# Kernel optimization log

Measured on AMD Instinct MI355X. Metric: run time of the kernel, lower is better.

## Reference

```python
import jax, jax.numpy as jnp
import numpy as np

D_MODEL, D_INNER, D_STATE, D_CONV, DT_RANK = 4, 8, 16, 4, 1


def _build_perms(N, H, W):
    # center-out 2D spatial order
    yy, xx = np.meshgrid(np.arange(H), np.arange(W), indexing='ij')
    cy, cx = H // 2, W // 2
    d2 = (yy - cy) ** 2 + (xx - cx) ** 2
    sp = np.argsort(d2.reshape(-1), kind='stable')          # (H*W,)
    HW = H * W
    # scanA: for each frame t, full center-out spatial sweep
    scanA = (np.arange(N)[:, None] * HW + sp[None, :]).reshape(-1)
    # scanB: for each spatial pos (in center-out order), zig-zag over frames
    fwd = np.arange(N)
    bwd = fwd[::-1]
    tids = np.where((np.arange(HW) % 2 == 0)[:, None], fwd[None, :], bwd[None, :])  # (HW, N)
    scanB = (tids * HW + sp[:, None]).reshape(-1)
    perms = np.stack([scanA, scanB, scanA[::-1], scanB[::-1]], axis=0)  # (4, L)
    return jnp.asarray(perms)


def _dwconv1d(x_bcl, w, b, pad, groups):
    # x: (B, C, L), w: (C, 1, K) depthwise
    y = jax.lax.conv_general_dilated(x_bcl, w, (1,), [pad],
                                     feature_group_count=groups,
                                     dimension_numbers=('NCH', 'OIH', 'NCH'))
    return y + b[None, :, None]


def _forward(x, dwconv_w, dwconv_b, in_proj_w, conv1d_w, conv1d_b,
             x_proj_w, dt_proj_w, dt_proj_b, A_log, Dp, out_proj_w, ln_g, ln_b):
    B, N, H, W = x.shape
    L = N * H * W
    perms = _build_perms(N, H, W)                 # (4, L) int, static
    xf = x.reshape(B, L)
    seqs = xf[:, perms]                            # (B, 4, L) gather along 4 scans
    seqs = _dwconv1d(seqs, dwconv_w, dwconv_b, (1, 1), 4)
    u = jax.nn.silu(seqs.transpose(0, 2, 1))       # (B, L, 4)
    # ---- Mamba(d_model=4) ----
    xz = jnp.einsum('bld,ed->ble', u, in_proj_w)   # (B, L, 2*d_inner)
    xm, z = xz[..., :D_INNER], xz[..., D_INNER:]
    xc = _dwconv1d(xm.transpose(0, 2, 1), conv1d_w, conv1d_b, (D_CONV - 1, 0), D_INNER)
    xm = jax.nn.silu(xc.transpose(0, 2, 1))        # (B, L, 8) causal conv + SiLU
    x_dbl = jnp.einsum('bld,ed->ble', xm, x_proj_w)  # (B, L, dt_rank+2*d_state)
    dt = x_dbl[..., :DT_RANK]
    Bm = x_dbl[..., DT_RANK:DT_RANK + D_STATE]     # (B, L, 16)
    Cm = x_dbl[..., DT_RANK + D_STATE:]            # (B, L, 16)
    dt = jax.nn.softplus(jnp.einsum('blr,dr->bld', dt, dt_proj_w) + dt_proj_b)  # (B, L, 8)
    A = -jnp.exp(A_log)                            # (8, 16)
    dA = jnp.exp(dt[..., None] * A)                # (B, L, 8, 16)
    dBx = dt[..., None] * Bm[:, :, None, :] * xm[..., None]  # (B, L, 8, 16)

    def step(h, inp):
        dA_t, dBx_t, C_t = inp
        h = dA_t * h + dBx_t                       # (B, 8, 16)
        return h, jnp.einsum('bds,bs->bd', h, C_t)

    h0 = jnp.zeros((B, D_INNER, D_STATE), x.dtype)
    _, ys = jax.lax.scan(step, h0, (dA.transpose(1, 0, 2, 3),
                                    dBx.transpose(1, 0, 2, 3),
                                    Cm.transpose(1, 0, 2)))
    y = ys.transpose(1, 0, 2) + xm * Dp            # (B, L, 8)
    y = y * jax.nn.silu(z)
    out = jnp.einsum('bld,ed->ble', y, out_proj_w)  # (B, L, 4)
    # ---- LayerNorm(4) ----
    mu = out.mean(-1, keepdims=True)
    var = ((out - mu) ** 2).mean(-1, keepdims=True)
    out = (out - mu) * jax.lax.rsqrt(var + 1e-5) * ln_g + ln_b
    # rec[:, inv[i]] = out[:, :, i]  <=>  rec_i = out[:, perms[i], i]
    rec = jnp.take_along_axis(out, perms.T[None], axis=1)  # (B, L, 4)
    return rec.mean(-1).reshape(B, N, H, W)


def setup_inputs() -> dict:
    key = jax.random.key(0)
    ks = jax.random.split(key, 12)
    s = 0.1
    x = jax.random.normal(ks[0], (4, 6, 128, 128), jnp.float32)
    return {
        'x': x,
        'dwconv_w': jax.random.normal(ks[1], (4, 1, 3), jnp.float32) * s,
        'dwconv_b': jnp.zeros((4,), jnp.float32),
        'in_proj_w': jax.random.normal(ks[2], (2 * D_INNER, D_MODEL), jnp.float32) * s,
        'conv1d_w': jax.random.normal(ks[3], (D_INNER, 1, D_CONV), jnp.float32) * s,
        'conv1d_b': jnp.zeros((D_INNER,), jnp.float32),
        'x_proj_w': jax.random.normal(ks[4], (DT_RANK + 2 * D_STATE, D_INNER), jnp.float32) * s,
        'dt_proj_w': jax.random.normal(ks[5], (D_INNER, DT_RANK), jnp.float32) * s,
        'dt_proj_b': jnp.full((D_INNER,), -2.0, jnp.float32),
        'A_log': jnp.log(jnp.tile(jnp.arange(1, D_STATE + 1, dtype=jnp.float32), (D_INNER, 1))),
        'Dp': jnp.ones((D_INNER,), jnp.float32),
        'out_proj_w': jax.random.normal(ks[6], (D_MODEL, D_INNER), jnp.float32) * s,
        'ln_g': jnp.ones((4,), jnp.float32),
        'ln_b': jnp.zeros((4,), jnp.float32),
    }


def reference(x, dwconv_w, dwconv_b, in_proj_w, conv1d_w, conv1d_b,
              x_proj_w, dt_proj_w, dt_proj_b, A_log, Dp, out_proj_w, ln_g, ln_b):
    return _forward(x, dwconv_w, dwconv_b, in_proj_w, conv1d_w, conv1d_b,
                    x_proj_w, dt_proj_w, dt_proj_b, A_log, Dp, out_proj_w, ln_g, ln_b)
```

## Files before the change

### kernel.cpp

```cpp
#include <hip/hip_runtime.h>
#include <math.h>

#define HWSZ  16384
#define LTOT  98304
#define NB    4
#define TCH   96
#define NCH   1024
#define GCH   64
#define NGRP  16
#define SD    100

__device__ __forceinline__ float siluf(float x){
  return x * __builtin_amdgcn_rcpf(1.f + __expf(-x));
}
__device__ __forceinline__ float softplusf(float x){
  return fmaxf(x, 0.f) + __logf(1.f + __expf(-fabsf(x)));
}

__device__ __forceinline__ float red16(float x){
  int v;
  v = __float_as_int(x);
  x += __int_as_float(__builtin_amdgcn_update_dpp(0, v, 0xB1, 0xF, 0xF, true));
  v = __float_as_int(x);
  x += __int_as_float(__builtin_amdgcn_update_dpp(0, v, 0x4E, 0xF, 0xF, true));
  v = __float_as_int(x);
  x += __int_as_float(__builtin_amdgcn_update_dpp(0, v, 0x141, 0xF, 0xF, true));
  v = __float_as_int(x);
  x += __int_as_float(__builtin_amdgcn_update_dpp(0, v, 0x140, 0xF, 0xF, true));
  return x;
}

__device__ __forceinline__ int rho0(int i, const int* __restrict__ sp){
  int n = i >> 14; int r = i & (HWSZ - 1);
  return (n << 14) + sp[r];
}
__device__ __forceinline__ int rho1(int i, const int* __restrict__ sp){
  unsigned ui = (unsigned)i;
  unsigned r = ui / 6u; unsigned n = ui - r * 6u;
  unsigned t = (r & 1u) ? (5u - n) : n;
  return (int)((t << 14) + (unsigned)sp[r]);
}

__global__ __launch_bounds__(256) void k_rank(int* __restrict__ sp){
  __shared__ int hist[8193];
  __shared__ int part[256];
  const int tid = threadIdx.x;
  for (int v = tid; v < 8193; v += 256) hist[v] = 0;
  __syncthreads();
  for (int jj = tid; jj < HWSZ; jj += 256){
    int dy = (jj >> 7) - 64, dx = (jj & 127) - 64;
    atomicAdd(&hist[dy*dy + dx*dx], 1);
  }
  __syncthreads();
  const int base = tid * 33;
  {
    int sum = 0;
    for (int m = 0; m < 33; ++m){ int v = base + m; if (v < 8193) sum += hist[v]; }
    part[tid] = sum;
  }
  __syncthreads();
  if (tid == 0){
    int run = 0;
    for (int t = 0; t < 256; ++t){ int c = part[t]; part[t] = run; run += c; }
  }
  __syncthreads();
  {
    int run = part[tid];
    for (int m = 0; m < 33; ++m){
      int v = base + m;
      if (v < 8193){ int c = hist[v]; hist[v] = run; run += c; }
    }
  }
  __syncthreads();

  const int j = blockIdx.x * 256 + tid;
  const int y = j >> 7, x = j & 127;
  const int dy = y - 64, dx = x - 64;
  const int v = dy*dy + dx*dx;
  int cnt = hist[v];
  const int r = __float2int_rd(sqrtf((float)v));
  int yp0 = 64 - r; if (yp0 < 0) yp0 = 0;
  int yp1 = 64 + r + 1; if (yp1 > y) yp1 = y;
  for (int yp = yp0; yp < yp1; ++yp){
    int dyp = yp - 64;
    int tt = v - dyp*dyp;
    int rr = __float2int_rn(sqrtf((float)tt));
    if (rr * rr == tt){
      cnt += (rr <= 64) ? 1 : 0;
      cnt += (rr >= 1 && rr <= 63) ? 1 : 0;
    }
  }
  if (x > 64) cnt += 1;
  sp[cnt] = j;
}

__global__ __launch_bounds__(128, 4)
void k_scan(const float* __restrict__ X,
            const float* __restrict__ dww, const float* __restrict__ dwb,
            const float* __restrict__ ipw,
            const float* __restrict__ c1w, const float* __restrict__ c1b,
            const float* __restrict__ xpw,
            const float* __restrict__ dtpw, const float* __restrict__ dtpb,
            const float* __restrict__ Alog,
            const int* __restrict__ sp,
            float* __restrict__ chA, float* __restrict__ chB,
            float* __restrict__ y0g, float4* __restrict__ ug4)
{
  const int c = blockIdx.x, b = blockIdx.y;
  const int c0 = c * TCH;
  const int tid = threadIdx.x;
  const float* Xb = X + (size_t)b * LTOT;

  __shared__ __align__(16) float s_pre[(TCH + 3) * 9];
  __shared__ __align__(16) float s_dt[8 * SD];
  __shared__ __align__(16) float s_dxm[8 * SD];
  __shared__ __align__(16) float s_Bv[16 * SD];
  __shared__ __align__(16) float s_Cv[16 * SD];

  if (tid < TCH + 3){
    const int m = tid;
    const int i = c0 - 3 + m;
    if (i < 0){
      #pragma unroll
      for (int d = 0; d < 8; ++d) s_pre[m*9 + d] = 0.f;
    } else {
      const int i2 = LTOT - 1 - i;
      const bool okm = (i > 0), okp = (i < LTOT - 1);
      int q[12];
      q[0]  = okm ? rho0(i - 1, sp) : 0;
      q[1]  =       rho0(i,     sp);
      q[2]  = okp ? rho0(i + 1, sp) : 0;
      q[3]  = okm ? rho1(i - 1, sp) : 0;
      q[4]  =       rho1(i,     sp);
      q[5]  = okp ? rho1(i + 1, sp) : 0;
      q[6]  = okm ? rho0(i2 + 1, sp) : 0;
      q[7]  =       rho0(i2,     sp);
      q[8]  = okp ? rho0(i2 - 1, sp) : 0;
      q[9]  = okm ? rho1(i2 + 1, sp) : 0;
      q[10] =       rho1(i2,     sp);
      q[11] = okp ? rho1(i2 - 1, sp) : 0;
      float xv[12];
      #pragma unroll
      for (int t = 0; t < 12; ++t) xv[t] = Xb[q[t]];
      if (!okm){ xv[0] = 0.f; xv[3] = 0.f; xv[6] = 0.f; xv[9]  = 0.f; }
      if (!okp){ xv[2] = 0.f; xv[5] = 0.f; xv[8] = 0.f; xv[11] = 0.f; }
      float u[4];
      #pragma unroll
      for (int k = 0; k < 4; ++k){
        float acc = dwb[k];
        acc = fmaf(dww[k*3+0], xv[k*3+0], acc);
        acc = fmaf(dww[k*3+1], xv[k*3+1], acc);
        acc = fmaf(dww[k*3+2], xv[k*3+2], acc);
        u[k] = siluf(acc);
      }
      ug4[(size_t)b * LTOT + i] = make_float4(u[0], u[1], u[2], u[3]);
      #pragma unroll
      for (int d = 0; d < 8; ++d){
        float acc =      ipw[d*4+0] * u[0];
        acc = fmaf(ipw[d*4+1], u[1], acc);
        acc = fmaf(ipw[d*4+2], u[2], acc);
        acc = fmaf(ipw[d*4+3], u[3], acc);
        s_pre[m*9 + d] = acc;
      }
    }
  }
  __syncthreads();

  if (tid < TCH){
    const int t = tid;
    float xm[8];
    #pragma unroll
    for (int d = 0; d < 8; ++d){
      float acc = c1b[d];
      #pragma unroll
      for (int tau = 0; tau < 4; ++tau)
        acc = fmaf(c1w[d*4+tau], s_pre[(t+tau)*9 + d], acc);
      xm[d] = siluf(acc);
    }
    float dtr = xpw[0] * xm[0];
    #pragma unroll
    for (int d = 1; d < 8; ++d) dtr = fmaf(xpw[d], xm[d], dtr);
    #pragma unroll
    for (int s = 0; s < 16; ++s){
      float acc = xpw[(1+s)*8] * xm[0];
      #pragma unroll
      for (int d = 1; d < 8; ++d) acc = fmaf(xpw[(1+s)*8+d], xm[d], acc);
      s_Bv[s*SD + t] = acc;
      float acc2 = xpw[(17+s)*8] * xm[0];
      #pragma unroll
      for (int d = 1; d < 8; ++d) acc2 = fmaf(xpw[(17+s)*8+d], xm[d], acc2);
      s_Cv[s*SD + t] = acc2;
    }
    #pragma unroll
    for (int d = 0; d < 8; ++d){
      float dtv = softplusf(fmaf(dtpw[d], dtr, dtpb[d]));
      s_dt[d*SD + t]  = dtv;
      s_dxm[d*SD + t] = dtv * xm[d];
    }
  }
  __syncthreads();

  {
    const int d = tid >> 4, s = tid & 15;
    const float Ads = -__expf(Alog[tid]);
    float h = 0.f, sdt = 0.f;
    const float* pdt = s_dt + d*SD;
    const float* pdx = s_dxm + d*SD;
    const float* pB  = s_Bv + s*SD;
    const float* pC  = s_Cv + s*SD;
    float* yb = y0g + ((size_t)b * NCH + c) * 768 + d * 96;
    for (int t0 = 0; t0 < TCH; t0 += 4){
      const float4 dt4 = *reinterpret_cast<const float4*>(pdt + t0);
      const float4 dx4 = *reinterpret_cast<const float4*>(pdx + t0);
      const float4 B4  = *reinterpret_cast<const float4*>(pB + t0);
      const float4 C4  = *reinterpret_cast<const float4*>(pC + t0);
      sdt += dt4.x + dt4.y + dt4.z + dt4.w;
      float y0, y1, y2, y3;
      { float dA = __expf(dt4.x*Ads); h = fmaf(dA, h, dx4.x*B4.x); y0 = h*C4.x; }
      { float dA = __expf(dt4.y*Ads); h = fmaf(dA, h, dx4.y*B4.y); y1 = h*C4.y; }
      { float dA = __expf(dt4.z*Ads); h = fmaf(dA, h, dx4.z*B4.z); y2 = h*C4.z; }
      { float dA = __expf(dt4.w*Ads); h = fmaf(dA, h, dx4.w*B4.w); y3 = h*C4.w; }
      y0 = red16(y0); y1 = red16(y1); y2 = red16(y2); y3 = red16(y3);
      if (s == 0)
        *reinterpret_cast<float4*>(yb + t0) = make_float4(y0, y1, y2, y3);
    }
    const size_t base = ((size_t)b * NCH + c) * 128 + tid;
    chA[base] = __expf(Ads * sdt);
    chB[base] = h;
  }
}

__global__ __launch_bounds__(128) void k_comb1(const float* __restrict__ chA,
                                               const float* __restrict__ chB,
                                               float* __restrict__ hpre,
                                               float* __restrict__ apre,
                                               float* __restrict__ GA,
                                               float* __restrict__ GB){
  const int j = blockIdx.x;
  const int g = j >> 2, b = j & 3;
  const int idx = threadIdx.x;
  const size_t base = ((size_t)b * NCH + (size_t)g * GCH) * 128 + idx;
  float h = 0.f, a = 1.f;
  float A_[8], B_[8];
  #pragma unroll
  for (int m = 0; m < 8; ++m){ A_[m] = chA[base + (size_t)m*128]; B_[m] = chB[base + (size_t)m*128]; }
  for (int cc = 0; cc < GCH; cc += 8){
    float A2[8], B2[8];
    if (cc + 8 < GCH){
      #pragma unroll
      for (int m = 0; m < 8; ++m){ A2[m] = chA[base + (size_t)(cc+8+m)*128]; B2[m] = chB[base + (size_t)(cc+8+m)*128]; }
    } else {
      #pragma unroll
      for (int m = 0; m < 8; ++m){ A2[m] = 0.f; B2[m] = 0.f; }
    }
    #pragma unroll
    for (int m = 0; m < 8; ++m){
      hpre[base + (size_t)(cc+m)*128] = h;
      apre[base + (size_t)(cc+m)*128] = a;
      h = fmaf(A_[m], h, B_[m]);
      a *= A_[m];
    }
    #pragma unroll
    for (int m = 0; m < 8; ++m){ A_[m] = A2[m]; B_[m] = B2[m]; }
  }
  GA[(size_t)(g*4+b)*128 + idx] = a;
  GB[(size_t)(g*4+b)*128 + idx] = h;
}

#define NBL (NB * LTOT)
__global__ __launch_bounds__(128, 4)
void k_corr(const float4* __restrict__ ug4,
            const float* __restrict__ ipw,
            const float* __restrict__ c1w, const float* __restrict__ c1b,
            const float* __restrict__ xpw,
            const float* __restrict__ dtpw, const float* __restrict__ dtpb,
            const float* __restrict__ Alog, const float* __restrict__ Dp,
            const float* __restrict__ opw,
            const float* __restrict__ lng, const float* __restrict__ lnb,
            const float* __restrict__ hpre, const float* __restrict__ apre,
            const float* __restrict__ GA, const float* __restrict__ GB,
            const float* __restrict__ y0g,
            float* __restrict__ outbuf)
{
  const int c = blockIdx.x, b = blockIdx.y;
  const int c0 = c * TCH;
  const int tid = threadIdx.x;
  const size_t cb = (size_t)b * NCH + c;

  __shared__ __align__(16) float s_pre[(TCH + 3) * 9];
  __shared__ __align__(16) float s_sg[8 * 104];
  __shared__ __align__(16) float s_xm[8 * 96];
  __shared__ __align__(16) float s_Ct[96 * 20];
  __shared__ __align__(16) float s_zs[8 * 96];
  __shared__ __align__(16) float s_hA[256];
  float* s_yf = s_pre;

  {
    const int g = c >> 6;
    const float hp = hpre[cb * 128 + tid];
    const float ap = apre[cb * 128 + tid];
    float Hv = 0.f;
    for (int gp = 0; gp < g; ++gp){
      const float ga = GA[(size_t)gp*512 + (size_t)b*128 + tid];
      const float gb = GB[(size_t)gp*512 + (size_t)b*128 + tid];
      Hv = fmaf(ga, Hv, gb);
    }
    s_hA[tid]       = fmaf(ap, Hv, hp);
    s_hA[128 + tid] = -__expf(Alog[tid]);
  }

  if (tid < TCH + 3){
    const int m = tid;
    const int i = c0 - 3 + m;
    if (i < 0){
      #pragma unroll
      for (int d = 0; d < 8; ++d) s_pre[m*9 + d] = 0.f;
    } else {
      const float4 u4 = ug4[(size_t)b * LTOT + i];
      const float u[4] = {u4.x, u4.y, u4.z, u4.w};
      #pragma unroll
      for (int d = 0; d < 8; ++d){
        float acc =      ipw[d*4+0] * u[0];
        acc = fmaf(ipw[d*4+1], u[1], acc);
        acc = fmaf(ipw[d*4+2], u[2], acc);
        acc = fmaf(ipw[d*4+3], u[3], acc);
        s_pre[m*9 + d] = acc;
      }
      if (m >= 3){
        const int t0 = m - 3;
        #pragma unroll
        for (int d = 0; d < 8; ++d){
          float acc =      ipw[(8+d)*4+0] * u[0];
          acc = fmaf(ipw[(8+d)*4+1], u[1], acc);
          acc = fmaf(ipw[(8+d)*4+2], u[2], acc);
          acc = fmaf(ipw[(8+d)*4+3], u[3], acc);
          s_zs[d*96 + t0] = siluf(acc);
        }
      }
    }
  }
  __syncthreads();

  if (tid < TCH){
    const int t = tid;
    float xm[8];
    #pragma unroll
    for (int d = 0; d < 8; ++d){
      float acc = c1b[d];
      #pragma unroll
      for (int tau = 0; tau < 4; ++tau)
        acc = fmaf(c1w[d*4+tau], s_pre[(t+tau)*9 + d], acc);
      float v = siluf(acc);
      xm[d] = v;
      s_xm[d*96 + t] = v;
    }
    float dtr = xpw[0] * xm[0];
    #pragma unroll
    for (int d = 1; d < 8; ++d) dtr = fmaf(xpw[d], xm[d], dtr);
    float* pct = s_Ct + t*20;
    #pragma unroll
    for (int s = 0; s < 16; ++s){
      float acc2 = xpw[(17+s)*8] * xm[0];
      #pragma unroll
      for (int d = 1; d < 8; ++d) acc2 = fmaf(xpw[(17+s)*8+d], xm[d], acc2);
      pct[s] = acc2;
    }
    #pragma unroll
    for (int d = 0; d < 8; ++d)
      s_sg[d*104 + t] = softplusf(fmaf(dtpw[d], dtr, dtpb[d]));
  }
  __syncthreads();

  if (tid < 8){
    float* ps = s_sg + tid*104;
    float run = 0.f;
    for (int t0 = 0; t0 < TCH; t0 += 4){
      const float4 d4 = *reinterpret_cast<const float4*>(ps + t0);
      float r0 = run + d4.x, r1 = r0 + d4.y, r2 = r1 + d4.z, r3 = r2 + d4.w;
      *reinterpret_cast<float4*>(ps + t0) = make_float4(r0, r1, r2, r3);
      run = r3;
    }
  }
  __syncthreads();

  {
    const int d = tid >> 4, tsub = tid & 15;
    float w[16], A16[16];
    #pragma unroll
    for (int s = 0; s < 16; ++s){
      w[s]   = s_hA[d*16 + s];
      A16[s] = s_hA[128 + d*16 + s];
    }
    const float* py0 = y0g + cb * 768 + d * 96;
    for (int t = tsub; t < TCH; t += 16){
      const float sg = s_sg[d*104 + t];
      float acc = py0[t];
      const float* pc = s_Ct + t*20;
      #pragma unroll
      for (int s4 = 0; s4 < 16; s4 += 4){
        const float4 C4 = *reinterpret_cast<const float4*>(pc + s4);
        acc = fmaf(C4.x, __expf(A16[s4+0]*sg) * w[s4+0], acc);
        acc = fmaf(C4.y, __expf(A16[s4+1]*sg) * w[s4+1], acc);
        acc = fmaf(C4.z, __expf(A16[s4+2]*sg) * w[s4+2], acc);
        acc = fmaf(C4.w, __expf(A16[s4+3]*sg) * w[s4+3], acc);
      }
      s_yf[d*96 + t] = acc;
    }
  }
  __syncthreads();

  if (tid < TCH){
    const int t = tid;
    const int i = c0 + t;
    float y[8];
    #pragma unroll
    for (int d = 0; d < 8; ++d)
      y[d] = (s_yf[d*96 + t] + s_xm[d*96 + t] * Dp[d]) * s_zs[d*96 + t];
    float o[4];
    #pragma unroll
    for (int e = 0; e < 4; ++e){
      float acc = opw[e*8] * y[0];
      #pragma unroll
      for (int d = 1; d < 8; ++d) acc = fmaf(opw[e*8+d], y[d], acc);
      o[e] = acc;
    }
    const float mu = 0.25f * (o[0] + o[1] + o[2] + o[3]);
    const float v0 = o[0] - mu, v1 = o[1] - mu, v2 = o[2] - mu, v3 = o[3] - mu;
    const float inv = rsqrtf(0.25f * (v0*v0 + v1*v1 + v2*v2 + v3*v3) + 1e-5f);
    const size_t base = (size_t)b * LTOT + i;
    outbuf[0*NBL + base] = fmaf(v0 * inv, lng[0], lnb[0]);
    outbuf[1*NBL + base] = fmaf(v1 * inv, lng[1], lnb[1]);
    outbuf[2*NBL + base] = fmaf(v2 * inv, lng[2], lnb[2]);
    outbuf[3*NBL + base] = fmaf(v3 * inv, lng[3], lnb[3]);
  }
}

__global__ __launch_bounds__(256) void k_final(const float* __restrict__ outbuf,
                                               const int* __restrict__ sp,
                                               float* __restrict__ out){
  const int l = blockIdx.x * 256 + threadIdx.x;
  const int b = blockIdx.y;
  const int q0 = rho0(l, sp), q1 = rho1(l, sp);
  const int j  = LTOT - 1 - l;
  const int q2 = rho0(j, sp), q3 = rho1(j, sp);
  const size_t pb = (size_t)b * LTOT;
  out[pb + l] = 0.25f * (outbuf[0*NBL + pb + q0] + outbuf[1*NBL + pb + q1] +
                         outbuf[2*NBL + pb + q2] + outbuf[3*NBL + pb + q3]);
}

extern "C" void kernel_launch(void* const* d_in, const int* in_sizes, int n_in,
                              void* d_out, int out_size, void* d_ws, size_t ws_size,
                              hipStream_t stream) {
  const float* X    = (const float*)d_in[0];
  const float* dww  = (const float*)d_in[1];
  const float* dwb  = (const float*)d_in[2];
  const float* ipw  = (const float*)d_in[3];
  const float* c1w  = (const float*)d_in[4];
  const float* c1b  = (const float*)d_in[5];
  const float* xpw  = (const float*)d_in[6];
  const float* dtpw = (const float*)d_in[7];
  const float* dtpb = (const float*)d_in[8];
  const float* Alog = (const float*)d_in[9];
  const float* Dp   = (const float*)d_in[10];
  const float* opw  = (const float*)d_in[11];
  const float* lng  = (const float*)d_in[12];
  const float* lnb  = (const float*)d_in[13];
  float* out = (float*)d_out;

  int* wsI    = (int*)d_ws;
  int* sp     = wsI;
  float* chA  = (float*)(wsI + 16384);
  float* chB  = chA  + 524288;
  float* hpre = chB  + 524288;
  float* apre = hpre + 524288;
  float* GA   = apre + 524288;
  float* GB   = GA + 8192;
  float4* ug4 = (float4*)(GB + 8192);
  float* y0g  = (float*)(ug4) + (size_t)NB * LTOT * 4;
  float* outbuf = y0g + 3145728;

  k_rank<<<64, 256, 0, stream>>>(sp);
  k_scan<<<dim3(NCH, NB), 128, 0, stream>>>(X, dww, dwb, ipw, c1w, c1b, xpw,
      dtpw, dtpb, Alog, sp, chA, chB, y0g, ug4);
  k_comb1<<<64, 128, 0, stream>>>(chA, chB, hpre, apre, GA, GB);
  k_corr<<<dim3(NCH, NB), 128, 0, stream>>>(ug4, ipw, c1w, c1b, xpw,
      dtpw, dtpb, Alog, Dp, opw, lng, lnb, hpre, apre, GA, GB, y0g, outbuf);
  k_final<<<dim3(LTOT / 256, NB), 256, 0, stream>>>(outbuf, sp, out);
}
```

Before: 184.4 us.

## Replace two-level chunk-carry combine with wave-parallel shuffle scan; histogram-free rank

The chunk-state combine now runs as one 64-lane wavefront scan per (batch, state) over 1024 chunks, using shuffle-based associative scans per segment with a carried prefix. It writes a single incoming-state array, so the correction kernel no longer loops over group prefixes or reads hpre/apre/GA/GB. The rank kernel drops its shared-memory histogram and prefix sum, counting smaller radii per thread with an integer-sqrt loop across 128 rows, and launches more blocks. This gives much more parallelism in the combine and less memory traffic, at the cost of more ALU work per thread in the rank kernel.

```diff
diff --git a/kernel.cpp b/kernel.cpp
--- a/kernel.cpp
+++ b/kernel.cpp
@@ -6,9 +6,8 @@
 #define NB    4
 #define TCH   96
 #define NCH   1024
-#define GCH   64
-#define NGRP  16
 #define SD    100
+#define NBL   (NB * LTOT)
 
 __device__ __forceinline__ float siluf(float x){
   return x * __builtin_amdgcn_rcpf(1.f + __expf(-x));
@@ -30,6 +29,13 @@
   return x;
 }
 
+__device__ __forceinline__ int isqrt_floor(int v){
+  int r = __float2int_rn(sqrtf((float)v));
+  if (r * r > v) --r;
+  else if ((r + 1) * (r + 1) <= v) ++r;
+  return r;
+}
+
 __device__ __forceinline__ int rho0(int i, const int* __restrict__ sp){
   int n = i >> 14; int r = i & (HWSZ - 1);
   return (n << 14) + sp[r];
@@ -41,56 +47,37 @@
   return (int)((t << 14) + (unsigned)sp[r]);
 }
 
-__global__ __launch_bounds__(256) void k_rank(int* __restrict__ sp){
-  __shared__ int hist[8193];
-  __shared__ int part[256];
-  const int tid = threadIdx.x;
-  for (int v = tid; v < 8193; v += 256) hist[v] = 0;
-  __syncthreads();
-  for (int jj = tid; jj < HWSZ; jj += 256){
-    int dy = (jj >> 7) - 64, dx = (jj & 127) - 64;
-    atomicAdd(&hist[dy*dy + dx*dx], 1);
-  }
-  __syncthreads();
-  const int base = tid * 33;
-  {
-    int sum = 0;
-    for (int m = 0; m < 33; ++m){ int v = base + m; if (v < 8193) sum += hist[v]; }
-    part[tid] = sum;
-  }
-  __syncthreads();
-  if (tid == 0){
-    int run = 0;
-    for (int t = 0; t < 256; ++t){ int c = part[t]; part[t] = run; run += c; }
-  }
-  __syncthreads();
-  {
-    int run = part[tid];
-    for (int m = 0; m < 33; ++m){
-      int v = base + m;
-      if (v < 8193){ int c = hist[v]; hist[v] = run; run += c; }
-    }
-  }
-  __syncthreads();
-
-  const int j = blockIdx.x * 256 + tid;
+__global__ __launch_bounds__(128) void k_rank(int* __restrict__ sp){
+  const int j = blockIdx.x * 128 + threadIdx.x;
   const int y = j >> 7, x = j & 127;
   const int dy = y - 64, dx = x - 64;
   const int v = dy*dy + dx*dx;
-  int cnt = hist[v];
-  const int r = __float2int_rd(sqrtf((float)v));
-  int yp0 = 64 - r; if (yp0 < 0) yp0 = 0;
-  int yp1 = 64 + r + 1; if (yp1 > y) yp1 = y;
-  for (int yp = yp0; yp < yp1; ++yp){
-    int dyp = yp - 64;
-    int tt = v - dyp*dyp;
-    int rr = __float2int_rn(sqrtf((float)tt));
-    if (rr * rr == tt){
-      cnt += (rr <= 64) ? 1 : 0;
-      cnt += (rr >= 1 && rr <= 63) ? 1 : 0;
-    }
-  }
-  if (x > 64) cnt += 1;
+  int cnt = 0;
+  for (int yy = 0; yy < 128; ++yy){
+    int dyy = yy - 64;
+    int w = v - dyy*dyy;
+    if (w > 0){
+      int m = isqrt_floor(w - 1);
+      int lo = m < 64 ? m : 64;
+      int hi = m < 63 ? m : 63;
+      cnt += lo + hi + 1;
+    }
+  }
+  {
+    const int r = isqrt_floor(v);
+    int yp0 = 64 - r; if (yp0 < 0) yp0 = 0;
+    int yp1 = 64 + r + 1; if (yp1 > y) yp1 = y;
+    for (int yp = yp0; yp < yp1; ++yp){
+      int dyp = yp - 64;
+      int tt = v - dyp*dyp;
+      int rr = isqrt_floor(tt);
+      if (rr * rr == tt){
+        cnt += (rr <= 64) ? 1 : 0;
+        cnt += (rr >= 1 && rr <= 63) ? 1 : 0;
+      }
+    }
+    if (x > 64) cnt += 1;
+  }
   sp[cnt] = j;
 }
 
@@ -230,44 +217,40 @@
   }
 }
 
-__global__ __launch_bounds__(128) void k_comb1(const float* __restrict__ chA,
-                                               const float* __restrict__ chB,
-                                               float* __restrict__ hpre,
-                                               float* __restrict__ apre,
-                                               float* __restrict__ GA,
-                                               float* __restrict__ GB){
-  const int j = blockIdx.x;
-  const int g = j >> 2, b = j & 3;
-  const int idx = threadIdx.x;
-  const size_t base = ((size_t)b * NCH + (size_t)g * GCH) * 128 + idx;
-  float h = 0.f, a = 1.f;
-  float A_[8], B_[8];
-  #pragma unroll
-  for (int m = 0; m < 8; ++m){ A_[m] = chA[base + (size_t)m*128]; B_[m] = chB[base + (size_t)m*128]; }
-  for (int cc = 0; cc < GCH; cc += 8){
-    float A2[8], B2[8];
-    if (cc + 8 < GCH){
-      #pragma unroll
-      for (int m = 0; m < 8; ++m){ A2[m] = chA[base + (size_t)(cc+8+m)*128]; B2[m] = chB[base + (size_t)(cc+8+m)*128]; }
-    } else {
-      #pragma unroll
-      for (int m = 0; m < 8; ++m){ A2[m] = 0.f; B2[m] = 0.f; }
-    }
-    #pragma unroll
-    for (int m = 0; m < 8; ++m){
-      hpre[base + (size_t)(cc+m)*128] = h;
-      apre[base + (size_t)(cc+m)*128] = a;
-      h = fmaf(A_[m], h, B_[m]);
-      a *= A_[m];
-    }
-    #pragma unroll
-    for (int m = 0; m < 8; ++m){ A_[m] = A2[m]; B_[m] = B2[m]; }
-  }
-  GA[(size_t)(g*4+b)*128 + idx] = a;
-  GB[(size_t)(g*4+b)*128 + idx] = h;
-}
-
-#define NBL (NB * LTOT)
+__global__ __launch_bounds__(128) void k_comb(const float* __restrict__ chA,
+                                              const float* __restrict__ chB,
+                                              float* __restrict__ hin){
+  const int wave = (blockIdx.x << 1) | (threadIdx.x >> 6);
+  const int lane = threadIdx.x & 63;
+  const int b   = wave >> 7;
+  const int idx = wave & 127;
+  const size_t basebi = (size_t)b * NCH * 128 + idx;
+  float carry = 0.f;
+  float a = chA[basebi + (size_t)lane * 128];
+  float h = chB[basebi + (size_t)lane * 128];
+  for (int seg = 0; seg < NCH / 64; ++seg){
+    float aN = 1.f, hN = 0.f;
+    if (seg + 1 < NCH / 64){
+      const size_t off = basebi + (size_t)((seg + 1) * 64 + lane) * 128;
+      aN = chA[off]; hN = chB[off];
+    }
+    #pragma unroll
+    for (int o = 1; o < 64; o <<= 1){
+      float aj = __shfl_up(a, o, 64);
+      float hj = __shfl_up(h, o, 64);
+      if (lane >= o){ h = fmaf(a, hj, h); a *= aj; }
+    }
+    float ae = __shfl_up(a, 1, 64);
+    float he = __shfl_up(h, 1, 64);
+    if (lane == 0){ ae = 1.f; he = 0.f; }
+    hin[basebi + (size_t)(seg * 64 + lane) * 128] = fmaf(ae, carry, he);
+    float aL = __shfl(a, 63, 64);
+    float hL = __shfl(h, 63, 64);
+    carry = fmaf(aL, carry, hL);
+    a = aN; h = hN;
+  }
+}
+
 __global__ __launch_bounds__(128, 4)
 void k_corr(const float4* __restrict__ ug4,
             const float* __restrict__ ipw,
@@ -277,8 +260,7 @@
             const float* __restrict__ Alog, const float* __restrict__ Dp,
             const float* __restrict__ opw,
             const float* __restrict__ lng, const float* __restrict__ lnb,
-            const float* __restrict__ hpre, const float* __restrict__ apre,
-            const float* __restrict__ GA, const float* __restrict__ GB,
+            const float* __restrict__ hin,
             const float* __restrict__ y0g,
             float* __restrict__ outbuf)
 {
@@ -295,19 +277,8 @@
   __shared__ __align__(16) float s_hA[256];
   float* s_yf = s_pre;
 
-  {
-    const int g = c >> 6;
-    const float hp = hpre[cb * 128 + tid];
-    const float ap = apre[cb * 128 + tid];
-    float Hv = 0.f;
-    for (int gp = 0; gp < g; ++gp){
-      const float ga = GA[(size_t)gp*512 + (size_t)b*128 + tid];
-      const float gb = GB[(size_t)gp*512 + (size_t)b*128 + tid];
-      Hv = fmaf(ga, Hv, gb);
-    }
-    s_hA[tid]       = fmaf(ap, Hv, hp);
-    s_hA[128 + tid] = -__expf(Alog[tid]);
-  }
+  s_hA[tid]       = hin[cb * 128 + tid];
+  s_hA[128 + tid] = -__expf(Alog[tid]);
 
   if (tid < TCH + 3){
     const int m = tid;
@@ -470,20 +441,17 @@
   int* wsI    = (int*)d_ws;
   int* sp     = wsI;
   float* chA  = (float*)(wsI + 16384);
-  float* chB  = chA  + 524288;
-  float* hpre = chB  + 524288;
-  float* apre = hpre + 524288;
-  float* GA   = apre + 524288;
-  float* GB   = GA + 8192;
-  float4* ug4 = (float4*)(GB + 8192);
+  float* chB  = chA + 524288;
+  float* hin  = chB + 524288;
+  float4* ug4 = (float4*)(hin + 524288);
   float* y0g  = (float*)(ug4) + (size_t)NB * LTOT * 4;
   float* outbuf = y0g + 3145728;
 
-  k_rank<<<64, 256, 0, stream>>>(sp);
+  k_rank<<<128, 128, 0, stream>>>(sp);
   k_scan<<<dim3(NCH, NB), 128, 0, stream>>>(X, dww, dwb, ipw, c1w, c1b, xpw,
       dtpw, dtpb, Alog, sp, chA, chB, y0g, ug4);
-  k_comb1<<<64, 128, 0, stream>>>(chA, chB, hpre, apre, GA, GB);
+  k_comb<<<256, 128, 0, stream>>>(chA, chB, hin);
   k_corr<<<dim3(NCH, NB), 128, 0, stream>>>(ug4, ipw, c1w, c1b, xpw,
-      dtpw, dtpb, Alog, Dp, opw, lng, lnb, hpre, apre, GA, GB, y0g, outbuf);
+      dtpw, dtpb, Alog, Dp, opw, lng, lnb, hin, y0g, outbuf);
   k_final<<<dim3(LTOT / 256, NB), 256, 0, stream>>>(outbuf, sp, out);
 }
```

New measurement: 197.0 us. 6.8% more time.
